# Optimization experiments

Hardware: AMD Instinct MI355X
Metric: run time of the kernel (lower is better)

Reference implementation:

```python
import jax, jax.numpy as jnp
from jax import lax
import numpy as np

WINDOW_SIZES = (1, 2, 3)


def _proj(x, w1, b1, w2, b2):
    # gated projection: sigmoid(Linear1) * tanh(Linear2)
    return jax.nn.sigmoid(x @ w1.T + b1) * jnp.tanh(x @ w2.T + b2)


def setup_inputs() -> dict:
    key = jax.random.key(0)
    ks = jax.random.split(key, 16)
    V, E, D = 50000, 1024, 1024
    N, La, Lq = 64, 512, 64
    s = 0.02  # weight scale to keep sigmoid/tanh unsaturated
    return {
        "data_q": jax.random.randint(ks[0], (Lq,), 0, V),
        "data_as": jax.random.randint(ks[1], (N, La), 0, V),
        "emb": jax.random.normal(ks[2], (V, E), jnp.float32),
        "w1": jax.random.normal(ks[3], (D, E), jnp.float32) * s,
        "b1": jnp.zeros((D,), jnp.float32),
        "w2": jax.random.normal(ks[4], (D, E), jnp.float32) * s,
        "b2": jnp.zeros((D,), jnp.float32),
        "cw1": jax.random.normal(ks[5], (D, D, 1), jnp.float32) * s,
        "cb1": jnp.zeros((D,), jnp.float32),
        "cw2": jax.random.normal(ks[6], (D, D, 2), jnp.float32) * s,
        "cb2": jnp.zeros((D,), jnp.float32),
        "cw3": jax.random.normal(ks[7], (D, D, 3), jnp.float32) * s,
        "cb3": jnp.zeros((D,), jnp.float32),
        "lin_w": jax.random.normal(ks[8], (D, 3 * D), jnp.float32) * s,
        "lin_b": jnp.zeros((D,), jnp.float32),
        "soft_w": jax.random.normal(ks[9], (1, D), jnp.float32) * s,
        "soft_b": jnp.zeros((1,), jnp.float32),
    }


def reference(data_q, data_as, emb, w1, b1, w2, b2,
              cw1, cb1, cw2, cb2, cw3, cb3, lin_w, lin_b, soft_w, soft_b):
    N, La = data_as.shape
    a_tok = data_as.reshape(-1)                     # [T] concatenated answers
    emb_a = emb[a_tok]                              # [T, E]
    emb_q = emb[data_q]                             # [Lq, E]
    pa = _proj(emb_a, w1, b1, w2, b2)               # [T, D]
    pq = _proj(emb_q, w1, b1, w2, b2)               # [Lq, D]

    # attention: M_r = q @ a^T ; alpha = softmax over question positions
    M = pq @ pa.T                                   # [Lq, T]
    alpha = jax.nn.softmax(M.T, axis=1)             # [T, Lq]
    Y = alpha @ pq                                  # [T, D]
    sim = pa * Y                                    # elementwise compare (mul)

    starts = jnp.arange(N) * La
    x = sim.T[None]                                 # [1, D, T]
    pools = []
    for w, cw, cb in zip(WINDOW_SIZES, (cw1, cw2, cw3), (cb1, cb2, cb3)):
        conv = lax.conv_general_dilated(
            x, cw, (1,), 'VALID',
            dimension_numbers=('NCW', 'OIW', 'NCW'))[0].T + cb  # [T-w+1, D]
        conv = jax.nn.relu(conv)
        # DMax: per-answer max over rows [start_k, start_k + La - w + 1)
        idx = starts[:, None] + jnp.arange(La - w + 1)[None, :]  # [N, La-w+1]
        pools.append(conv[idx].max(axis=1))          # [N, D]

    cat = jnp.concatenate(pools, axis=1)            # [N, 3D]
    h = jnp.tanh(cat @ lin_w.T + lin_b)             # [N, D]
    logits = (h @ soft_w.T + soft_b).reshape(-1)    # [N]
    return jax.nn.log_softmax(logits)
```

## Files before the change

kernel.cpp:

```cpp
#include <hip/hip_runtime.h>

#define DEV __device__ __forceinline__

typedef __bf16 bf16x8 __attribute__((ext_vector_type(8)));
typedef float f32x4 __attribute__((ext_vector_type(4)));
typedef unsigned short u16;
typedef u16 u16x4 __attribute__((ext_vector_type(4)));

constexpr int T_ANS = 32768;
constexpr int LQ    = 64;
constexpr int M_ALL = T_ANS + LQ;
constexpr int M_PAD = 33024;
constexpr int DIM   = 1024;

DEV u16 f2bf(float x) {
  unsigned u = __float_as_uint(x);
  return (u16)((u + 0x7FFFu + ((u >> 16) & 1u)) >> 16);
}
DEV float bf2f(u16 s) { return __uint_as_float(((unsigned)s) << 16); }

DEV void gl2lds16(const void* g, void* l) {
  __builtin_amdgcn_global_load_lds(
      (const __attribute__((address_space(1))) unsigned int*)g,
      (__attribute__((address_space(3))) unsigned int*)l, 16, 0, 0);
}

#define MF(A, B, C) __builtin_amdgcn_mfma_f32_16x16x32_bf16(A, B, C, 0, 0, 0)
#define LFC(P, OFF) (*(const bf16x8*)((P) + (OFF)))


#define STG(G, LT, R0) gl2lds16((G) + (R0) * 2048 + gOff, (LT) + (R0) * 64 + ldOff)

#define S_TILE(AT, BT, BUF)                                                           \
  { const char* ga_ = (AT); const char* gb_ = (BT); char* lb_ = (BUF);                \
    STG(ga_, lb_, 0); STG(ga_, lb_, 128);                                             \
    STG(gb_, lb_ + 16384, 0); STG(gb_, lb_ + 16384, 128); }

#define VMC4 asm volatile("s_waitcnt vmcnt(4)" ::: "memory");
#define VMC0 asm volatile("s_waitcnt vmcnt(0)" ::: "memory");

#define TILEV3(BUF, STAGES, WAIT)                                                     \
  {                                                                                   \
    STAGES                                                                            \
    const char* Ar = (BUF) + rdA;                                                     \
    const char* Br = (BUF) + 16384 + rdB;                                             \
    bf16x8 a0 = LFC(Ar, 0),    a1 = LFC(Ar, 1024), a2 = LFC(Ar, 2048), a3 = LFC(Ar, 3072); \
    bf16x8 a4 = LFC(Ar, 4096), a5 = LFC(Ar, 5120), a6 = LFC(Ar, 6144), a7 = LFC(Ar, 7168); \
    bf16x8 c0 = LFC(Br, 0), c1 = LFC(Br, 1024), c2 = LFC(Br, 2048), c3 = LFC(Br, 3072);    \
    acc[0][0] = MF(a0, c0, acc[0][0]); acc[0][1] = MF(a0, c1, acc[0][1]);             \
    acc[0][2] = MF(a0, c2, acc[0][2]); acc[0][3] = MF(a0, c3, acc[0][3]);             \
    acc[1][0] = MF(a1, c0, acc[1][0]); acc[1][1] = MF(a1, c1, acc[1][1]);             \
    acc[1][2] = MF(a1, c2, acc[1][2]); acc[1][3] = MF(a1, c3, acc[1][3]);             \
    acc[2][0] = MF(a2, c0, acc[2][0]); acc[2][1] = MF(a2, c1, acc[2][1]);             \
    acc[2][2] = MF(a2, c2, acc[2][2]); acc[2][3] = MF(a2, c3, acc[2][3]);             \
    acc[3][0] = MF(a3, c0, acc[3][0]); acc[3][1] = MF(a3, c1, acc[3][1]);             \
    acc[3][2] = MF(a3, c2, acc[3][2]); acc[3][3] = MF(a3, c3, acc[3][3]);             \
    acc[4][0] = MF(a4, c0, acc[4][0]); acc[4][1] = MF(a4, c1, acc[4][1]);             \
    acc[4][2] = MF(a4, c2, acc[4][2]); acc[4][3] = MF(a4, c3, acc[4][3]);             \
    acc[5][0] = MF(a5, c0, acc[5][0]); acc[5][1] = MF(a5, c1, acc[5][1]);             \
    acc[5][2] = MF(a5, c2, acc[5][2]); acc[5][3] = MF(a5, c3, acc[5][3]);             \
    acc[6][0] = MF(a6, c0, acc[6][0]); acc[6][1] = MF(a6, c1, acc[6][1]);             \
    acc[6][2] = MF(a6, c2, acc[6][2]); acc[6][3] = MF(a6, c3, acc[6][3]);             \
    acc[7][0] = MF(a7, c0, acc[7][0]); acc[7][1] = MF(a7, c1, acc[7][1]);             \
    acc[7][2] = MF(a7, c2, acc[7][2]); acc[7][3] = MF(a7, c3, acc[7][3]);             \
    WAIT                                                                              \
    asm volatile("s_barrier" ::: "memory");                                           \
  }

#define GEMM_V3(NT)                                                                   \
  f32x4 acc[8][4] = {};                                                               \
  const int ldOff = tid * 16;                                                         \
  const int gOff = (tid >> 2) * 2048 + (((tid & 3) ^ ((tid >> 2) & 3)) << 4);         \
  const int blk_ = (((lane >> 4) ^ (lane & 3)) << 4);                                 \
  const int rdA = (wm + (lane & 15)) * 64 + blk_;                                     \
  const int rdB = (wn + (lane & 15)) * 64 + blk_;                                     \
  char* b0_ = lds; char* b1_ = lds + 32768; char* b2_ = lds + 65536; char* b3_ = lds + 98304; \
  S_TILE(Ab(0), Bb(0), b0_) S_TILE(Ab(1), Bb(1), b1_)                                 \
  VMC4                                                                                \
  asm volatile("s_barrier" ::: "memory");                                             \
  for (int g = 0; g < (NT) / 4 - 1; ++g) {                                            \
    const int t = 4 * g;                                                              \
    TILEV3(b0_, S_TILE(Ab(t + 2), Bb(t + 2), b2_), VMC4)                              \
    TILEV3(b1_, S_TILE(Ab(t + 3), Bb(t + 3), b3_), VMC4)                              \
    TILEV3(b2_, S_TILE(Ab(t + 4), Bb(t + 4), b0_), VMC4)                              \
    TILEV3(b3_, S_TILE(Ab(t + 5), Bb(t + 5), b1_), VMC4)                              \
  }                                                                                   \
  {                                                                                   \
    const int t = (NT) - 4;                                                           \
    TILEV3(b0_, S_TILE(Ab(t + 2), Bb(t + 2), b2_), VMC4)                              \
    TILEV3(b1_, S_TILE(Ab(t + 3), Bb(t + 3), b3_), VMC4)                              \
    TILEV3(b2_, , VMC0)                                                               \
    TILEV3(b3_, , )                                                                   \
  }


__global__ void cast4(const float* __restrict__ src, u16* __restrict__ dst, int n4) {
  int i = blockIdx.x * 256 + threadIdx.x;
  if (i < n4) {
    float4 v = ((const float4*)src)[i];
    u16x4 o = { f2bf(v.x), f2bf(v.y), f2bf(v.z), f2bf(v.w) };
    ((u16x4*)dst)[i] = o;
  }
}

template<int W>
__global__ void cast_conv_w(const float* __restrict__ src, u16* __restrict__ dst) {
  int i = blockIdx.x * 256 + threadIdx.x;
  if (i < 1024 * 1024) {
#pragma unroll
    for (int k = 0; k < W; ++k)
      dst[(size_t)k * (1024 * 1024) + i] = f2bf(src[(size_t)i * W + k]);
  }
}

__global__ void pack_w12(const float* __restrict__ w1, const float* __restrict__ w2,
                         u16* __restrict__ W12) {
  int i = blockIdx.x * 256 + threadIdx.x;
  if (i < 2048 * 1024) {
    int n2 = i >> 10, k = i & 1023;
    int j = n2 >> 4, m = n2 & 15;
    const float* src = (j & 1) ? w2 : w1;
    W12[i] = f2bf(src[(size_t)((j >> 1) * 16 + m) * 1024 + k]);
  }
}

__global__ void gather_cast(const int* __restrict__ dq, const int* __restrict__ das,
                            const float* __restrict__ emb, u16* __restrict__ X) {
  const int row = blockIdx.x;
  const int c   = threadIdx.x;
  size_t dsto = (size_t)row * DIM + c * 4;
  if (row >= M_ALL) {
    u16x4 z = {0, 0, 0, 0};
    *(u16x4*)(X + dsto) = z;
    return;
  }
  const int tok = (row < T_ANS) ? das[row] : dq[row - T_ANS];
  float4 v = ((const float4*)(emb + (size_t)tok * DIM))[c];
  u16x4 o = { f2bf(v.x), f2bf(v.y), f2bf(v.z), f2bf(v.w) };
  *(u16x4*)(X + dsto) = o;
}

__global__ void transpose_pq(const u16* __restrict__ pa, u16* __restrict__ pqT) {
  int i = blockIdx.x * 256 + threadIdx.x;
  int e = i >> 6, q = i & 63;
  pqT[i] = pa[(size_t)(T_ANS + q) * DIM + e];
}

__global__ void zero_pad_sim(u16* __restrict__ sim) {
  int i = blockIdx.x * 256 + threadIdx.x;
  if (i < 2 * DIM) sim[(size_t)T_ANS * DIM + i] = 0;
}

__global__ void cast_cat(const float* __restrict__ cat, u16* __restrict__ catb) {
  int i = blockIdx.x * 256 + threadIdx.x;
  if (i < 128 * 3072) {
    int row = i / 3072;
    catb[i] = (row < 64) ? f2bf(cat[i]) : (u16)0;
  }
}


__global__ __launch_bounds__(256)
void proj_g(const u16* __restrict__ X, const u16* __restrict__ W12,
            const float* __restrict__ b1, const float* __restrict__ b2,
            u16* __restrict__ pa) {
  __shared__ alignas(16) u16 sA[128 * 32];
  __shared__ alignas(16) u16 sB[128 * 32];
  const int tid = threadIdx.x, lane = tid & 63;
  const int wid = tid >> 6;
  const int wm = (wid >> 1) * 64, wn = (wid & 1) * 64;
  const int wg = ((int)blockIdx.x % 8) * 516 + (int)blockIdx.x / 8;
  const int tm = (wg >> 4) * 128, tn = (wg & 15) * 128;
  f32x4 acc[4][4] = {};
  for (int k0 = 0; k0 < 1024; k0 += 32) {
#pragma unroll
    for (int j = 0; j < 2; ++j) {
      const int f = tid * 16 + j * 4096;
      const int r = f >> 6, cb = f & 63;
      gl2lds16((const char*)X   + (size_t)(tm + r) * 2048 + k0 * 2 + cb, (char*)sA + f);
      gl2lds16((const char*)W12 + (size_t)(tn + r) * 2048 + k0 * 2 + cb, (char*)sB + f);
    }
    __syncthreads();
    const int lr = lane & 15, lk = (lane >> 4) * 8;
    bf16x8 af[4], bf[4];
#pragma unroll
    for (int i = 0; i < 4; ++i) {
      af[i] = *(const bf16x8*)(sA + (wm + i * 16 + lr) * 32 + lk);
      bf[i] = *(const bf16x8*)(sB + (wn + i * 16 + lr) * 32 + lk);
    }
#pragma unroll
    for (int mi = 0; mi < 4; ++mi)
#pragma unroll
      for (int ni = 0; ni < 4; ++ni)
        acc[mi][ni] = MF(af[mi], bf[ni], acc[mi][ni]);
    __syncthreads();
  }
  const int lr = lane & 15, lg = (lane >> 4) * 4;
#pragma unroll
  for (int np = 0; np < 2; ++np) {
    const int col = ((tn + wn) >> 1) + np * 16 + lr;
    const float b1v = b1[col], b2v = b2[col];
#pragma unroll
    for (int mi = 0; mi < 4; ++mi)
#pragma unroll
      for (int r = 0; r < 4; ++r) {
        const int row = tm + wm + mi * 16 + lg + r;
        const float x1 = acc[mi][2 * np][r] + b1v;
        const float x2 = acc[mi][2 * np + 1][r] + b2v;
        const float sg = 1.f / (1.f + __expf(-x1));
        const float th = 2.f / (1.f + __expf(-2.f * x2)) - 1.f;
        pa[(size_t)row * DIM + col] = f2bf(sg * th);
      }
  }
}


template<int W>
__global__ __launch_bounds__(512, 1)
void conv_g(const u16* __restrict__ sim, const u16* __restrict__ Bw,
            const float* __restrict__ cb, float* __restrict__ cat) {
  extern __shared__ char lds[];
  const int tid = threadIdx.x, lane = tid & 63;
  const int wid = tid >> 6;
  const int wm = (wid >> 2) * 128, wn = (wid & 3) * 64;
  const int lr = lane & 15;
  const int wg = ((int)blockIdx.x % 8) * 64 + (int)blockIdx.x / 8;
  const int tm = (wg >> 2) * 256, tn = (wg & 3) * 256;
  const char* Ag = (const char*)sim + (size_t)tm * 2048;
  const char* Bg = (const char*)Bw + (size_t)tn * 2048;
  auto Ab = [&](int t) { return Ag + (t >> 5) * 2048 + ((t & 31) << 6); };
  auto Bb = [&](int t) { return Bg + (size_t)(t >> 5) * 2097152 + ((t & 31) << 6); };

  GEMM_V3(32 * W)

  const int lg = (lane >> 4) * 4;
  const int n = tm >> 9;
#pragma unroll
  for (int ni = 0; ni < 4; ++ni) {
    const int col = tn + wn + ni * 16 + lr;
    const float cbv = cb[col];
    float vmax = 0.f;
#pragma unroll
    for (int mi = 0; mi < 8; ++mi)
#pragma unroll
      for (int r = 0; r < 4; ++r) {
        const int t = tm + wm + mi * 16 + lg + r;
        float v = fmaxf(acc[mi][ni][r] + cbv, 0.f);
        if ((t & 511) > 512 - W) v = 0.f;
        vmax = fmaxf(vmax, v);
      }
    vmax = fmaxf(vmax, __shfl_xor(vmax, 16));
    vmax = fmaxf(vmax, __shfl_xor(vmax, 32));
    if (lane < 16)
      atomicMax((int*)&cat[(size_t)n * 3072 + (W - 1) * 1024 + col], __float_as_int(vmax));
  }
}


__global__ __launch_bounds__(256, 2)
void attn_s(const u16* __restrict__ pa, float* __restrict__ Spart) {
  __shared__ alignas(16) u16 sA[128 * 32];
  __shared__ alignas(16) u16 sB[64 * 32];
  const int tid = threadIdx.x, lane = tid & 63;
  const int tm = blockIdx.x * 128;
  const int kbase = blockIdx.y * 256;
  const int wid = tid >> 6;
  const int wm = (wid >> 1) * 64, wn = (wid & 1) * 32;
  const u16* pq = pa + (size_t)T_ANS * DIM;
  f32x4 acc[4][2] = {};
  for (int k0 = kbase; k0 < kbase + 256; k0 += 32) {
#pragma unroll
    for (int j = 0; j < 2; ++j) {
      const int f = tid * 16 + j * 4096;
      const int r = f >> 6, cb = f & 63;
      gl2lds16((const char*)pa + (size_t)(tm + r) * 2048 + k0 * 2 + cb, (char*)sA + f);
    }
    {
      const int f = tid * 16;
      const int r = f >> 6, cb = f & 63;
      gl2lds16((const char*)pq + (size_t)r * 2048 + k0 * 2 + cb, (char*)sB + f);
    }
    __syncthreads();
    const int lr = lane & 15, lk = (lane >> 4) * 8;
    bf16x8 af[4], bfr[2];
#pragma unroll
    for (int i = 0; i < 4; ++i)
      af[i] = *(const bf16x8*)(sA + (wm + i * 16 + lr) * 32 + lk);
#pragma unroll
    for (int i = 0; i < 2; ++i)
      bfr[i] = *(const bf16x8*)(sB + (wn + i * 16 + lr) * 32 + lk);
#pragma unroll
    for (int mi = 0; mi < 4; ++mi)
#pragma unroll
      for (int ni = 0; ni < 2; ++ni)
        acc[mi][ni] = MF(af[mi], bfr[ni], acc[mi][ni]);
    __syncthreads();
  }
  const int lr = lane & 15, lg = (lane >> 4) * 4;
  float* Sp = Spart + (size_t)blockIdx.y * (T_ANS * 64);
#pragma unroll
  for (int mi = 0; mi < 4; ++mi)
#pragma unroll
    for (int ni = 0; ni < 2; ++ni)
#pragma unroll
      for (int r = 0; r < 4; ++r) {
        const int row = tm + wm + mi * 16 + lg + r;
        const int col = wn + ni * 16 + lr;
        Sp[(size_t)row * 64 + col] = acc[mi][ni][r];
      }
}

__global__ void softmax64(const float* __restrict__ Spart, u16* __restrict__ alpha) {
  const int row = blockIdx.x * 4 + (threadIdx.x >> 6);
  const int lane = threadIdx.x & 63;
  const size_t o = (size_t)row * 64 + lane;
  float v = Spart[o] + Spart[(size_t)1 * T_ANS * 64 + o]
          + Spart[(size_t)2 * T_ANS * 64 + o] + Spart[(size_t)3 * T_ANS * 64 + o];
  float m = v;
#pragma unroll
  for (int o2 = 32; o2 > 0; o2 >>= 1) m = fmaxf(m, __shfl_xor(m, o2));
  const float e = __expf(v - m);
  float s = e;
#pragma unroll
  for (int o2 = 32; o2 > 0; o2 >>= 1) s += __shfl_xor(s, o2);
  alpha[(size_t)row * 64 + lane] = f2bf(e / s);
}


__global__ __launch_bounds__(256, 2)
void attn_y_sim(const u16* __restrict__ alpha, const u16* __restrict__ pqT,
                const u16* __restrict__ pa, u16* __restrict__ sim) {
  __shared__ alignas(16) u16 sA[128 * 32];
  __shared__ alignas(16) u16 sB[128 * 32];
  const int tid = threadIdx.x, lane = tid & 63;
  const int tm = blockIdx.x * 128, tn = blockIdx.y * 128;
  const int wid = tid >> 6;
  const int wm = (wid >> 1) * 64, wn = (wid & 1) * 64;
  f32x4 acc[4][4] = {};
  for (int k0 = 0; k0 < 64; k0 += 32) {
#pragma unroll
    for (int j = 0; j < 2; ++j) {
      const int f = tid * 16 + j * 4096;
      const int r = f >> 6, cb = f & 63;
      gl2lds16((const char*)alpha + (size_t)(tm + r) * 128 + k0 * 2 + cb, (char*)sA + f);
      gl2lds16((const char*)pqT   + (size_t)(tn + r) * 128 + k0 * 2 + cb, (char*)sB + f);
    }
    __syncthreads();
    const int lr = lane & 15, lk = (lane >> 4) * 8;
    bf16x8 af[4], bfr[4];
#pragma unroll
    for (int i = 0; i < 4; ++i) {
      af[i]  = *(const bf16x8*)(sA + (wm + i * 16 + lr) * 32 + lk);
      bfr[i] = *(const bf16x8*)(sB + (wn + i * 16 + lr) * 32 + lk);
    }
#pragma unroll
    for (int mi = 0; mi < 4; ++mi)
#pragma unroll
      for (int ni = 0; ni < 4; ++ni)
        acc[mi][ni] = MF(af[mi], bfr[ni], acc[mi][ni]);
    __syncthreads();
  }
  const int lr = lane & 15, lg = (lane >> 4) * 4;
#pragma unroll
  for (int ni = 0; ni < 4; ++ni) {
    const int col = tn + wn + ni * 16 + lr;
#pragma unroll
    for (int mi = 0; mi < 4; ++mi)
#pragma unroll
      for (int r = 0; r < 4; ++r) {
        const int row = tm + wm + mi * 16 + lg + r;
        const size_t o = (size_t)row * DIM + col;
        sim[o] = f2bf(bf2f(pa[o]) * acc[mi][ni][r]);
      }
  }
}


__global__ __launch_bounds__(256, 2)
void final_h(const u16* __restrict__ catb, const u16* __restrict__ linb,
             const float* __restrict__ lin_b, float* __restrict__ h) {
  __shared__ alignas(16) u16 sA[128 * 32];
  __shared__ alignas(16) u16 sB[128 * 32];
  const int tid = threadIdx.x, lane = tid & 63;
  const int tn = blockIdx.y * 128;
  const int wid = tid >> 6;
  const int wm = (wid >> 1) * 64, wn = (wid & 1) * 64;
  f32x4 acc[4][4] = {};
  for (int k0 = 0; k0 < 3072; k0 += 32) {
#pragma unroll
    for (int j = 0; j < 2; ++j) {
      const int f = tid * 16 + j * 4096;
      const int r = f >> 6, cb = f & 63;
      gl2lds16((const char*)catb + (size_t)r * 6144 + k0 * 2 + cb, (char*)sA + f);
      gl2lds16((const char*)linb + (size_t)(tn + r) * 6144 + k0 * 2 + cb, (char*)sB + f);
    }
    __syncthreads();
    const int lr = lane & 15, lk = (lane >> 4) * 8;
    bf16x8 af[4], bfr[4];
#pragma unroll
    for (int i = 0; i < 4; ++i) {
      af[i]  = *(const bf16x8*)(sA + (wm + i * 16 + lr) * 32 + lk);
      bfr[i] = *(const bf16x8*)(sB + (wn + i * 16 + lr) * 32 + lk);
    }
#pragma unroll
    for (int mi = 0; mi < 4; ++mi)
#pragma unroll
      for (int ni = 0; ni < 4; ++ni)
        acc[mi][ni] = MF(af[mi], bfr[ni], acc[mi][ni]);
    __syncthreads();
  }
  const int lr = lane & 15, lg = (lane >> 4) * 4;
#pragma unroll
  for (int ni = 0; ni < 4; ++ni) {
    const int col = tn + wn + ni * 16 + lr;
    const float bv = lin_b[col];
#pragma unroll
    for (int mi = 0; mi < 4; ++mi)
#pragma unroll
      for (int r = 0; r < 4; ++r) {
        const int row = wm + mi * 16 + lg + r;
        if (row < 64) {
          const float x = acc[mi][ni][r] + bv;
          h[(size_t)row * DIM + col] = 2.f / (1.f + __expf(-2.f * x)) - 1.f;
        }
      }
  }
}

__global__ void final_logits(const float* __restrict__ h, const float* __restrict__ soft_w,
                             const float* __restrict__ soft_b, float* __restrict__ out) {
  __shared__ float part[256];
  const int t = threadIdx.x;
  const int n = t >> 2, q = t & 3;
  float s = 0.f;
  for (int j = q * 256; j < q * 256 + 256; ++j) s += h[(size_t)n * DIM + j] * soft_w[j];
  part[t] = s;
  __syncthreads();
  if (t < 64) {
    float logit = part[t * 4] + part[t * 4 + 1] + part[t * 4 + 2] + part[t * 4 + 3] + soft_b[0];
    float m = logit;
#pragma unroll
    for (int o = 32; o > 0; o >>= 1) m = fmaxf(m, __shfl_xor(m, o));
    float e = __expf(logit - m);
    float ssum = e;
#pragma unroll
    for (int o = 32; o > 0; o >>= 1) ssum += __shfl_xor(ssum, o);
    out[t] = (logit - m) - logf(ssum);
  }
}


extern "C" void kernel_launch(void* const* d_in, const int* in_sizes, int n_in,
                              void* d_out, int out_size, void* d_ws, size_t ws_size,
                              hipStream_t stream) {
  const int*   data_q  = (const int*)d_in[0];
  const int*   data_as = (const int*)d_in[1];
  const float* emb     = (const float*)d_in[2];
  const float* w1      = (const float*)d_in[3];
  const float* b1      = (const float*)d_in[4];
  const float* w2      = (const float*)d_in[5];
  const float* b2      = (const float*)d_in[6];
  const float* cw1     = (const float*)d_in[7];
  const float* cb1     = (const float*)d_in[8];
  const float* cw2     = (const float*)d_in[9];
  const float* cb2     = (const float*)d_in[10];
  const float* cw3     = (const float*)d_in[11];
  const float* cb3     = (const float*)d_in[12];
  const float* lin_w   = (const float*)d_in[13];
  const float* lin_b   = (const float*)d_in[14];
  const float* soft_w  = (const float*)d_in[15];
  const float* soft_b  = (const float*)d_in[16];
  float* out = (float*)d_out;

  hipFuncSetAttribute((const void*)conv_g<1>, hipFuncAttributeMaxDynamicSharedMemorySize, 131072);
  hipFuncSetAttribute((const void*)conv_g<2>, hipFuncAttributeMaxDynamicSharedMemorySize, 131072);
  hipFuncSetAttribute((const void*)conv_g<3>, hipFuncAttributeMaxDynamicSharedMemorySize, 131072);

  u16* X     = (u16*)d_ws;
  u16* pa    = X    + (size_t)M_PAD * DIM;
  u16* W12   = pa   + (size_t)M_PAD * DIM;
  u16* cwb   = W12  + (size_t)2 * 1024 * 1024;
  u16* linb  = cwb  + (size_t)6 * 1024 * 1024;
  u16* pqT   = linb + (size_t)3 * 1024 * 1024;
  u16* alpha = pqT  + 64 * 1024;
  float* cat = (float*)(alpha + (size_t)T_ANS * 64);
  u16* catb  = (u16*)(cat + 64 * 3072);
  float* h   = (float*)(catb + 128 * 3072);
  u16* simb  = X;
  float* Spart = (float*)X;

  hipMemsetAsync(cat, 0, 64 * 3072 * sizeof(float), stream);

  pack_w12<<<8192, 256, 0, stream>>>(w1, w2, W12);
  cast4<<<3072, 256, 0, stream>>>(lin_w, linb, 3072 * 1024 / 4);
  cast_conv_w<1><<<4096, 256, 0, stream>>>(cw1, cwb);
  cast_conv_w<2><<<4096, 256, 0, stream>>>(cw2, cwb + (size_t)1 * 1024 * 1024);
  cast_conv_w<3><<<4096, 256, 0, stream>>>(cw3, cwb + (size_t)3 * 1024 * 1024);

  gather_cast<<<M_PAD, 256, 0, stream>>>(data_q, data_as, emb, X);

  proj_g<<<4128, 256, 0, stream>>>(X, W12, b1, b2, pa);
  transpose_pq<<<256, 256, 0, stream>>>(pa, pqT);

  attn_s<<<dim3(T_ANS / 128, 4), 256, 0, stream>>>(pa, Spart);
  softmax64<<<T_ANS / 4, 256, 0, stream>>>(Spart, alpha);
  attn_y_sim<<<dim3(T_ANS / 128, 8), 256, 0, stream>>>(alpha, pqT, pa, simb);
  zero_pad_sim<<<8, 256, 0, stream>>>(simb);

  conv_g<1><<<512, 512, 131072, stream>>>(simb, cwb, cb1, cat);
  conv_g<2><<<512, 512, 131072, stream>>>(simb, cwb + (size_t)1 * 1024 * 1024, cb2, cat);
  conv_g<3><<<512, 512, 131072, stream>>>(simb, cwb + (size_t)3 * 1024 * 1024, cb3, cat);

  cast_cat<<<1536, 256, 0, stream>>>(cat, catb);
  final_h<<<dim3(1, 8), 256, 0, stream>>>(catb, linb, lin_b, h);
  final_logits<<<1, 256, 0, stream>>>(h, soft_w, soft_b, out);
}
```

Baseline: 759.1 us.

## Rewrite projection GEMM with 256-row tiles, 4-stage LDS pipeline and fused gated epilogue

The answer-side projection GEMM moves from a small 128x128 tile kernel with single-buffered LDS to the large 256x256 tile, 4-stage global_load_lds pipelined core used by the conv kernels. Each persistent block walks four 256-column segments in turn and applies the sigmoid*tanh epilogue after each. The 64 question rows go to a separate small kernel. The LDS swizzle gains an extra XOR term to cut bank conflicts, and MFMA sections are wrapped in s_setprio to favour math waves. The intent is more operand reuse per loaded byte and better latency hiding. It runs only 256 blocks of 512 threads with 128KB LDS, so occupancy is one block per CU.

```diff
diff --git a/kernel.cpp b/kernel.cpp
--- a/kernel.cpp
+++ b/kernel.cpp
@@ -42,6 +42,7 @@
 #define TILEV3(BUF, STAGES, WAIT)                                                     \
   {                                                                                   \
     STAGES                                                                            \
+    __builtin_amdgcn_s_setprio(1);                                                    \
     const char* Ar = (BUF) + rdA;                                                     \
     const char* Br = (BUF) + 16384 + rdB;                                             \
     bf16x8 a0 = LFC(Ar, 0),    a1 = LFC(Ar, 1024), a2 = LFC(Ar, 2048), a3 = LFC(Ar, 3072); \
@@ -63,28 +64,33 @@
     acc[6][2] = MF(a6, c2, acc[6][2]); acc[6][3] = MF(a6, c3, acc[6][3]);             \
     acc[7][0] = MF(a7, c0, acc[7][0]); acc[7][1] = MF(a7, c1, acc[7][1]);             \
     acc[7][2] = MF(a7, c2, acc[7][2]); acc[7][3] = MF(a7, c3, acc[7][3]);             \
+    __builtin_amdgcn_s_setprio(0);                                                    \
     WAIT                                                                              \
     asm volatile("s_barrier" ::: "memory");                                           \
   }
 
+#define CORE_BASES                                                                    \
+  const int ldOff = tid * 16;                                                         \
+  const int gOff = (tid >> 2) * 2048 +                                                \
+      ((((tid & 3) ^ ((tid >> 2) & 3) ^ ((tid >> 4) & 3))) << 4);                     \
+  const int blk_ = (((lane >> 4) ^ (lane & 3) ^ ((lane >> 2) & 3)) << 4);             \
+  const int rdA = (wm + (lane & 15)) * 64 + blk_;                                     \
+  const int rdB = (wn + (lane & 15)) * 64 + blk_;                                     \
+  char* b0_ = lds; char* b1_ = lds + 32768; char* b2_ = lds + 65536; char* b3_ = lds + 98304;
+
+#define GROUP4(T0)                                                                    \
+    TILEV3(b0_, S_TILE(Ab((T0) + 2), Bb((T0) + 2), b2_), VMC4)                        \
+    TILEV3(b1_, S_TILE(Ab((T0) + 3), Bb((T0) + 3), b3_), VMC4)                        \
+    TILEV3(b2_, S_TILE(Ab((T0) + 4), Bb((T0) + 4), b0_), VMC4)                        \
+    TILEV3(b3_, S_TILE(Ab((T0) + 5), Bb((T0) + 5), b1_), VMC4)
+
 #define GEMM_V3(NT)                                                                   \
   f32x4 acc[8][4] = {};                                                               \
-  const int ldOff = tid * 16;                                                         \
-  const int gOff = (tid >> 2) * 2048 + (((tid & 3) ^ ((tid >> 2) & 3)) << 4);         \
-  const int blk_ = (((lane >> 4) ^ (lane & 3)) << 4);                                 \
-  const int rdA = (wm + (lane & 15)) * 64 + blk_;                                     \
-  const int rdB = (wn + (lane & 15)) * 64 + blk_;                                     \
-  char* b0_ = lds; char* b1_ = lds + 32768; char* b2_ = lds + 65536; char* b3_ = lds + 98304; \
+  CORE_BASES                                                                          \
   S_TILE(Ab(0), Bb(0), b0_) S_TILE(Ab(1), Bb(1), b1_)                                 \
   VMC4                                                                                \
   asm volatile("s_barrier" ::: "memory");                                             \
-  for (int g = 0; g < (NT) / 4 - 1; ++g) {                                            \
-    const int t = 4 * g;                                                              \
-    TILEV3(b0_, S_TILE(Ab(t + 2), Bb(t + 2), b2_), VMC4)                              \
-    TILEV3(b1_, S_TILE(Ab(t + 3), Bb(t + 3), b3_), VMC4)                              \
-    TILEV3(b2_, S_TILE(Ab(t + 4), Bb(t + 4), b0_), VMC4)                              \
-    TILEV3(b3_, S_TILE(Ab(t + 5), Bb(t + 5), b1_), VMC4)                              \
-  }                                                                                   \
+  for (int g = 0; g < (NT) / 4 - 1; ++g) { GROUP4(4 * g) }                            \
   {                                                                                   \
     const int t = (NT) - 4;                                                           \
     TILEV3(b0_, S_TILE(Ab(t + 2), Bb(t + 2), b2_), VMC4)                              \
@@ -160,17 +166,80 @@
 }
 
 
-__global__ __launch_bounds__(256)
+__global__ __launch_bounds__(512, 1)
 void proj_g(const u16* __restrict__ X, const u16* __restrict__ W12,
             const float* __restrict__ b1, const float* __restrict__ b2,
             u16* __restrict__ pa) {
+  extern __shared__ char lds[];
+  const int tid = threadIdx.x, lane = tid & 63;
+  const int wid = tid >> 6;
+  const int wm = (wid >> 2) * 128, wn = (wid & 3) * 64;
+  const int lr = lane & 15, lg = (lane >> 4) * 4;
+  const int wg = ((int)blockIdx.x % 8) * 32 + (int)blockIdx.x / 8;
+  const int tm = (wg & 127) * 256, tnh = wg >> 7;
+  const char* Ag = (const char*)X + (size_t)tm * 2048;
+  const char* Bg = (const char*)W12 + (size_t)tnh * 2097152;
+  auto Ab = [&](int t) { return Ag + ((t & 31) << 6); };
+  auto Bb = [&](int t) { return Bg + (size_t)(t >> 5) * 524288 + ((t & 31) << 6); };
+
+  f32x4 acc[8][4] = {};
+  CORE_BASES
+
+  auto epi = [&](int seg) {
+    const int colbase = (tnh * 4 + seg) * 128;
+#pragma unroll
+    for (int pp = 0; pp < 2; ++pp) {
+      const int clocal = ((wn >> 5) + pp) * 16 + lr;
+      const int col = colbase + clocal;
+      const float b1v = b1[col], b2v = b2[col];
+#pragma unroll
+      for (int mi = 0; mi < 8; ++mi)
+#pragma unroll
+        for (int r = 0; r < 4; ++r) {
+          const int row = tm + wm + mi * 16 + lg + r;
+          const float x1 = acc[mi][2 * pp][r] + b1v;
+          const float x2 = acc[mi][2 * pp + 1][r] + b2v;
+          const float sg = 1.f / (1.f + __expf(-x1));
+          const float th = 2.f / (1.f + __expf(-2.f * x2)) - 1.f;
+          pa[(size_t)row * DIM + col] = f2bf(sg * th);
+        }
+    }
+#pragma unroll
+    for (int i = 0; i < 8; ++i)
+#pragma unroll
+      for (int j = 0; j < 4; ++j) acc[i][j] = (f32x4){0.f, 0.f, 0.f, 0.f};
+  };
+
+  S_TILE(Ab(0), Bb(0), b0_) S_TILE(Ab(1), Bb(1), b1_)
+  VMC4
+  asm volatile("s_barrier" ::: "memory");
+#pragma unroll 1
+  for (int seg = 0; seg < 3; ++seg) {
+    for (int g = 0; g < 8; ++g) { GROUP4(seg * 32 + 4 * g) }
+    epi(seg);
+  }
+  for (int g = 0; g < 7; ++g) { GROUP4(96 + 4 * g) }
+  {
+    TILEV3(b0_, S_TILE(Ab(126), Bb(126), b2_), VMC4)
+    TILEV3(b1_, S_TILE(Ab(127), Bb(127), b3_), VMC4)
+    TILEV3(b2_, , VMC0)
+    TILEV3(b3_, , )
+  }
+  epi(3);
+}
+
+
+__global__ __launch_bounds__(256)
+void proj_pq(const u16* __restrict__ X, const u16* __restrict__ W12,
+             const float* __restrict__ b1, const float* __restrict__ b2,
+             u16* __restrict__ pa) {
   __shared__ alignas(16) u16 sA[128 * 32];
   __shared__ alignas(16) u16 sB[128 * 32];
   const int tid = threadIdx.x, lane = tid & 63;
   const int wid = tid >> 6;
   const int wm = (wid >> 1) * 64, wn = (wid & 1) * 64;
-  const int wg = ((int)blockIdx.x % 8) * 516 + (int)blockIdx.x / 8;
-  const int tm = (wg >> 4) * 128, tn = (wg & 15) * 128;
+  const int tm = T_ANS;
+  const int tn = (int)blockIdx.x * 128;
   f32x4 acc[4][4] = {};
   for (int k0 = 0; k0 < 1024; k0 += 32) {
 #pragma unroll
@@ -472,6 +541,7 @@
   const float* soft_b  = (const float*)d_in[16];
   float* out = (float*)d_out;
 
+  hipFuncSetAttribute((const void*)proj_g, hipFuncAttributeMaxDynamicSharedMemorySize, 131072);
   hipFuncSetAttribute((const void*)conv_g<1>, hipFuncAttributeMaxDynamicSharedMemorySize, 131072);
   hipFuncSetAttribute((const void*)conv_g<2>, hipFuncAttributeMaxDynamicSharedMemorySize, 131072);
   hipFuncSetAttribute((const void*)conv_g<3>, hipFuncAttributeMaxDynamicSharedMemorySize, 131072);
@@ -499,7 +569,8 @@
 
   gather_cast<<<M_PAD, 256, 0, stream>>>(data_q, data_as, emb, X);
 
-  proj_g<<<4128, 256, 0, stream>>>(X, W12, b1, b2, pa);
+  proj_pq<<<16, 256, 0, stream>>>(X, W12, b1, b2, pa);
+  proj_g<<<256, 512, 131072, stream>>>(X, W12, b1, b2, pa);
   transpose_pq<<<256, 256, 0, stream>>>(pa, pqT);
 
   attn_s<<<dim3(T_ANS / 128, 4), 256, 0, stream>>>(pa, Spart);
```

Measured after the change: 839.5 us. +10.6%, slower.
